# Performance work log

Measured on AMD Instinct MI355X. Metric: run time of the kernel, lower is better.

Reference implementation:

```python
import jax, jax.numpy as jnp
import numpy as np

N_AA = 300000
N_PROT = 30000
D_AA = 128
D_PROT = 128
HID = 128
OUT = 64
E_AP = 300000
E_PP = 960000
BATCH = 16384
NEG_SLOPE = 0.2


def _gatv2(x_src, x_dst, src, dst, Wl, bl, Wr, br, att, bias, num_dst):
    # GATv2Conv (heads=1): e_ij = att . leaky_relu(Wl x_j + Wr x_i); softmax over dst; out_i = sum alpha_ij * (Wl x_j) + bias
    xl = x_src @ Wl + bl                      # [Ns, C]
    xr = x_dst @ Wr + br                      # [Nd, C]
    e = jax.nn.leaky_relu(xl[src] + xr[dst], NEG_SLOPE)   # [E, C]
    logits = e @ att                          # [E]
    lmax = jax.ops.segment_max(logits, dst, num_segments=num_dst)
    ex = jnp.exp(logits - lmax[dst])
    denom = jax.ops.segment_sum(ex, dst, num_segments=num_dst)
    alpha = ex / denom[dst]                   # [E]
    msg = xl[src] * alpha[:, None]            # [E, C]
    out = jax.ops.segment_sum(msg, dst, num_segments=num_dst)
    return out + bias


def setup_inputs() -> dict:
    key = jax.random.key(0)
    ks = jax.random.split(key, 16)
    s = 0.05
    x_aa = jax.random.normal(ks[0], (N_AA, D_AA), jnp.float32)
    x_prot = jax.random.normal(ks[1], (N_PROT, D_PROT), jnp.float32)
    edge_index_ap = jnp.stack([
        jax.random.randint(ks[2], (E_AP,), 0, N_AA),
        jax.random.randint(ks[3], (E_AP,), 0, N_PROT)])
    edge_index_pp = jnp.stack([
        jax.random.randint(ks[4], (E_PP,), 0, N_PROT),
        jax.random.randint(ks[5], (E_PP,), 0, N_PROT)])
    return {
        'x_aa': x_aa, 'x_prot': x_prot,
        'edge_index_ap': edge_index_ap, 'edge_index_pp': edge_index_pp,
        'batch_size': BATCH,
        'Wl_ap': s * jax.random.normal(ks[6], (D_AA, HID), jnp.float32),
        'bl_ap': jnp.zeros((HID,), jnp.float32),
        'Wr_ap': s * jax.random.normal(ks[7], (D_PROT, HID), jnp.float32),
        'br_ap': jnp.zeros((HID,), jnp.float32),
        'att_ap': s * jax.random.normal(ks[8], (HID,), jnp.float32),
        'bias_ap': jnp.zeros((HID,), jnp.float32),
        'Wl_pp': s * jax.random.normal(ks[9], (D_PROT, HID), jnp.float32),
        'bl_pp': jnp.zeros((HID,), jnp.float32),
        'Wr_pp': s * jax.random.normal(ks[10], (D_PROT, HID), jnp.float32),
        'br_pp': jnp.zeros((HID,), jnp.float32),
        'att_pp': s * jax.random.normal(ks[11], (HID,), jnp.float32),
        'bias_pp': jnp.zeros((HID,), jnp.float32),
        'W_lin': s * jax.random.normal(ks[12], (HID, OUT), jnp.float32),
        'b_lin': jnp.zeros((OUT,), jnp.float32),
    }


def reference(x_aa, x_prot, edge_index_ap, edge_index_pp, batch_size,
              Wl_ap, bl_ap, Wr_ap, br_ap, att_ap, bias_ap,
              Wl_pp, bl_pp, Wr_pp, br_pp, att_pp, bias_pp,
              W_lin, b_lin):
    out_ap = _gatv2(x_aa, x_prot, edge_index_ap[0], edge_index_ap[1],
                    Wl_ap, bl_ap, Wr_ap, br_ap, att_ap, bias_ap, N_PROT)
    out_pp = _gatv2(x_prot, x_prot, edge_index_pp[0], edge_index_pp[1],
                    Wl_pp, bl_pp, Wr_pp, br_pp, att_pp, bias_pp, N_PROT)
    x = out_ap + out_pp                      # HeteroConv aggr='sum'
    x = jax.nn.relu(x[:batch_size])
    return x @ W_lin + b_lin
```

## Files before the change

kernel.cpp:

```cpp
#include <hip/hip_runtime.h>
#include <hip/hip_bf16.h>

typedef __attribute__((ext_vector_type(8))) short short8;
typedef __attribute__((ext_vector_type(4))) unsigned short ushort4_t;
typedef __attribute__((ext_vector_type(4))) float f32x4;

#define CAP_AP 64
#define CAP_PP 128

__device__ __forceinline__ unsigned short f2bf(float f) {
  unsigned u = __float_as_uint(f);
  u += 0x7FFFu + ((u >> 16) & 1u);
  return (unsigned short)(u >> 16);
}

__global__ __launch_bounds__(256) void k_init(
    int* __restrict__ map, int* __restrict__ cnt_ap, int* __restrict__ cnt_pp,
    int* __restrict__ ccount, int n_aa, int batch)
{
  int i = blockIdx.x * 256 + threadIdx.x;
  if (i < n_aa) map[i] = -1;
  if (i < batch) { cnt_ap[i] = 0; cnt_pp[i] = 0; }
  if (i == 0) *ccount = 0;
}

__global__ __launch_bounds__(256) void k_edges(
    const int* __restrict__ ei_ap, const int* __restrict__ ei_pp,
    int* __restrict__ map, int* __restrict__ cnt_ap, int* __restrict__ cnt_pp,
    int* __restrict__ csr_ap, int* __restrict__ csr_pp,
    int e_ap, int e_pp, int nb_ap, int batch)
{
  int b = blockIdx.x;
  if (b < nb_ap) {
    int e = b * 256 + threadIdx.x;
    if (e < e_ap) {
      int d = ei_ap[e_ap + e];
      if (d < batch) {
        int s = ei_ap[e];
        int pos = atomicAdd(&cnt_ap[d], 1);
        if (pos < CAP_AP) csr_ap[d * CAP_AP + pos] = s;
        map[s] = 1;
      }
    }
  } else {
    int e = (b - nb_ap) * 256 + threadIdx.x;
    if (e < e_pp) {
      int d = ei_pp[e_pp + e];
      if (d < batch) {
        int pos = atomicAdd(&cnt_pp[d], 1);
        if (pos < CAP_PP) csr_pp[d * CAP_PP + pos] = ei_pp[e];
      }
    }
  }
}

__global__ __launch_bounds__(256) void k_assign(
    int* __restrict__ map, int* __restrict__ inv, int* __restrict__ ccount, int n)
{
  __shared__ int wb[4];
  int i = blockIdx.x * 256 + threadIdx.x;
  bool need = (i < n) && (map[i] == 1);
  unsigned long long m = __ballot(need);
  int wave = threadIdx.x >> 6;
  int lane = threadIdx.x & 63;
  if (lane == 0) wb[wave] = __popcll(m);
  __syncthreads();
  if (threadIdx.x == 0) {
    int t0 = wb[0], t1 = wb[1], t2 = wb[2], t3 = wb[3];
    int tot = t0 + t1 + t2 + t3;
    int base = tot ? atomicAdd(ccount, tot) : 0;
    wb[0] = base;
    wb[1] = base + t0;
    wb[2] = base + t0 + t1;
    wb[3] = base + t0 + t1 + t2;
  }
  __syncthreads();
  if (need) {
    int slot = wb[wave] + __popcll(m & ((1ull << lane) - 1ull));
    map[i] = slot;
    inv[slot] = i;
  }
}

struct GemmJob {
  const float* X; const int* inv; const int* rowsp; int M;
  const float* W; const float* bias; unsigned short* Y; int nb;
};

__device__ __forceinline__ void gemm_body(const GemmJob& J, int bid, short8* lwb)
{
  const int tid = threadIdx.x;
  const int rows = J.rowsp ? *J.rowsp : J.M;
  const int wave = tid >> 6;
  const int lane = tid & 63;
  const int quad = lane >> 4;
  const int l16  = lane & 15;

  int tile = bid;
  long xrow = -1;
  float4 xa[4], xb[4];
  {
    int ra = tile * 64 + wave * 16 + l16;
    if (ra < rows) xrow = J.inv ? (long)J.inv[ra] : (long)ra;
    if (xrow >= 0) {
#pragma unroll
      for (int kt = 0; kt < 4; ++kt) {
        const float* p = J.X + xrow * 128 + kt * 32 + quad * 8;
        xa[kt] = ((const float4*)p)[0];
        xb[kt] = ((const float4*)p)[1];
      }
    }
  }

  {
    unsigned short* lw16 = (unsigned short*)lwb;
#pragma unroll
    for (int p = 0; p < 16; ++p) {
      int fi = p * 1024 + tid * 4;
      float4 w4 = *(const float4*)(J.W + fi);
#pragma unroll
      for (int q = 0; q < 4; ++q) {
        int k = (fi + q) >> 7, n = (fi + q) & 127;
        float wv = (q == 0) ? w4.x : (q == 1) ? w4.y : (q == 2) ? w4.z : w4.w;
        int e = ((k >> 5) * 8 + (n >> 4)) * 64 + ((k >> 3) & 3) * 16 + (n & 15);
        e ^= (e >> 6) & 7;
        lw16[e * 8 + (k & 7)] = f2bf(wv);
      }
    }
  }
  __syncthreads();

  for (; tile * 64 < rows; tile += J.nb) {
    int ra = tile * 64 + wave * 16 + l16;
    if (tile != bid) {
      xrow = -1;
      if (ra < rows) xrow = J.inv ? (long)J.inv[ra] : (long)ra;
      if (xrow >= 0) {
#pragma unroll
        for (int kt = 0; kt < 4; ++kt) {
          const float* p = J.X + xrow * 128 + kt * 32 + quad * 8;
          xa[kt] = ((const float4*)p)[0];
          xb[kt] = ((const float4*)p)[1];
        }
      }
    }

    short8 xf[4];
#pragma unroll
    for (int kt = 0; kt < 4; ++kt) {
      short8 a = {};
      if (xrow >= 0) {
        a[0] = (short)f2bf(xa[kt].x); a[1] = (short)f2bf(xa[kt].y);
        a[2] = (short)f2bf(xa[kt].z); a[3] = (short)f2bf(xa[kt].w);
        a[4] = (short)f2bf(xb[kt].x); a[5] = (short)f2bf(xb[kt].y);
        a[6] = (short)f2bf(xb[kt].z); a[7] = (short)f2bf(xb[kt].w);
      }
      xf[kt] = a;
    }

    f32x4 accs[8];
#pragma unroll
    for (int nt = 0; nt < 8; ++nt) {
      f32x4 acc = {0.f, 0.f, 0.f, 0.f};
#pragma unroll
      for (int kt = 0; kt < 4; ++kt)
        acc = __builtin_amdgcn_mfma_f32_16x16x32_bf16(
            lwb[(kt * 8 + nt) * 64 + (lane ^ nt)], xf[kt], acc, 0, 0, 0);
      accs[nt] = acc;
    }

    if (ra < rows) {
      unsigned short* yp = J.Y + (long)ra * 128;
#pragma unroll
      for (int nt = 0; nt < 8; ++nt) {
        int col = nt * 16 + quad * 4;
        float4 bv = *(const float4*)(J.bias + col);
        ushort4_t v;
        v[0] = f2bf(accs[nt][0] + bv.x);
        v[1] = f2bf(accs[nt][1] + bv.y);
        v[2] = f2bf(accs[nt][2] + bv.z);
        v[3] = f2bf(accs[nt][3] + bv.w);
        *(ushort4_t*)(yp + col) = v;
      }
    }
  }
}

__global__ __launch_bounds__(256) void k_mega(
    GemmJob j0, GemmJob j1, GemmJob j2, GemmJob j3,
    const int* __restrict__ map, const int* __restrict__ cnt_ap,
    int* __restrict__ csr_ap, int nb_gemm, int nb_remap, int batch)
{
  __shared__ short8 lwb[4 * 8 * 64];
  int b = blockIdx.x;
  if (b < nb_gemm) {
    if (b < j0.nb)                      gemm_body(j0, b, lwb);
    else if (b < j0.nb + j1.nb)         gemm_body(j1, b - j0.nb, lwb);
    else if (b < j0.nb + j1.nb + j2.nb) gemm_body(j2, b - j0.nb - j1.nb, lwb);
    else                                gemm_body(j3, b - j0.nb - j1.nb - j2.nb, lwb);
  } else {
    int i = (b - nb_gemm) * 256 + threadIdx.x;
    if (i < batch * CAP_AP) {
      int d = i / CAP_AP;
      int slot = i - d * CAP_AP;
      int n = cnt_ap[d]; if (n > CAP_AP) n = CAP_AP;
      if (slot < n) csr_ap[i] = map[csr_ap[i]];
    }
  }
}

__global__ __launch_bounds__(256) void k_gat_final(
    const int* __restrict__ cnt_ap, const int* __restrict__ csr_ap,
    const unsigned short* __restrict__ xl_aa,
    const unsigned short* __restrict__ xr_ap, const float* __restrict__ att_ap,
    const int* __restrict__ cnt_pp, const int* __restrict__ csr_pp,
    const unsigned short* __restrict__ xl_pp,
    const unsigned short* __restrict__ xr_pp, const float* __restrict__ att_pp,
    const float* __restrict__ bias_ap, const float* __restrict__ bias_pp,
    const float* __restrict__ W_lin, const float* __restrict__ b_lin,
    float* __restrict__ out, int batch)
{
  __shared__ unsigned lw2[64 * 64];
  __shared__ float lh[4][128];
  for (int e = threadIdx.x; e < 4096; e += 256) {
    int cp = e >> 6, o = e & 63;
    unsigned lo = f2bf(W_lin[(2 * cp) * 64 + o]);
    unsigned hi = f2bf(W_lin[(2 * cp + 1) * 64 + o]);
    lw2[e] = lo | (hi << 16);
  }

  const int wave = threadIdx.x >> 6;
  const int lane = threadIdx.x & 63;
  const int g    = lane >> 4;
  const int l16  = lane & 15;
  const int cb   = l16 * 8;
  const int dst  = blockIdx.x * 4 + wave;

  float h[8];
  if (dst < batch) {
    {
      float4 ba0 = *(const float4*)(bias_ap + cb);
      float4 ba1 = *(const float4*)(bias_ap + cb + 4);
      float4 bp0 = *(const float4*)(bias_pp + cb);
      float4 bp1 = *(const float4*)(bias_pp + cb + 4);
      h[0] = ba0.x + bp0.x; h[1] = ba0.y + bp0.y;
      h[2] = ba0.z + bp0.z; h[3] = ba0.w + bp0.w;
      h[4] = ba1.x + bp1.x; h[5] = ba1.y + bp1.y;
      h[6] = ba1.z + bp1.z; h[7] = ba1.w + bp1.w;
    }

#pragma unroll
    for (int type = 0; type < 2; ++type) {
      const int* cnt  = type ? cnt_pp : cnt_ap;
      const int* csr  = type ? csr_pp : csr_ap;
      const int cap   = type ? CAP_PP : CAP_AP;
      const unsigned short* xl = type ? xl_pp : xl_aa;
      const unsigned short* xr = type ? xr_pp : xr_ap;
      const float* att = type ? att_pp : att_ap;

      int n = __builtin_amdgcn_readfirstlane(cnt[dst]);
      if (n > cap) n = cap;
      const long base = (long)dst * cap;

      float xrv[8], atv[8];
      {
        short8 uxr = *(const short8*)(xr + (long)dst * 128 + cb);
#pragma unroll
        for (int k = 0; k < 8; ++k)
          xrv[k] = __uint_as_float(((unsigned)(unsigned short)uxr[k]) << 16);
        float4 a0 = *(const float4*)(att + cb);
        float4 a1 = *(const float4*)(att + cb + 4);
        atv[0] = a0.x; atv[1] = a0.y; atv[2] = a0.z; atv[3] = a0.w;
        atv[4] = a1.x; atv[5] = a1.y; atv[6] = a1.z; atv[7] = a1.w;
      }

      float l = 0.f, o[8];
#pragma unroll
      for (int k = 0; k < 8; ++k) o[k] = 0.f;

      if (n > 0) {
        bool act = g < n;
        int si = act ? csr[base + g] : 0;
        short8 ua = *(const short8*)(xl + (long)si * 128 + cb);
        int niter = (n + 3) >> 2;
        for (int it = 0; it < niter; ++it) {
          int en = it * 4 + 4 + g;
          bool actn = en < n;
          int sin = actn ? csr[base + en] : 0;
          short8 uan = *(const short8*)(xl + (long)sin * 128 + cb);

          float a[8];
#pragma unroll
          for (int k = 0; k < 8; ++k)
            a[k] = __uint_as_float(((unsigned)(unsigned short)ua[k]) << 16);
          float p = 0.f;
#pragma unroll
          for (int k = 0; k < 8; ++k) {
            float e = a[k] + xrv[k];
            e = e > 0.f ? e : 0.2f * e;
            p = fmaf(atv[k], e, p);
          }
          p += __shfl_xor(p, 8, 64);
          p += __shfl_xor(p, 4, 64);
          p += __shfl_xor(p, 2, 64);
          p += __shfl_xor(p, 1, 64);
          float w = act ? __expf(p) : 0.f;
          l += w;
#pragma unroll
          for (int k = 0; k < 8; ++k) o[k] = fmaf(w, a[k], o[k]);

          ua = uan; act = actn;
        }
      }
      l += __shfl_xor(l, 16, 64);
      l += __shfl_xor(l, 32, 64);
#pragma unroll
      for (int k = 0; k < 8; ++k) {
        o[k] += __shfl_xor(o[k], 16, 64);
        o[k] += __shfl_xor(o[k], 32, 64);
      }
      float invl = (l > 0.f) ? 1.f / l : 0.f;
#pragma unroll
      for (int k = 0; k < 8; ++k) h[k] = fmaf(o[k], invl, h[k]);
    }
  } else {
#pragma unroll
    for (int k = 0; k < 8; ++k) h[k] = 0.f;
  }

  if (g == 0) {
    float4 r0, r1;
    r0.x = h[0] > 0.f ? h[0] : 0.f; r0.y = h[1] > 0.f ? h[1] : 0.f;
    r0.z = h[2] > 0.f ? h[2] : 0.f; r0.w = h[3] > 0.f ? h[3] : 0.f;
    r1.x = h[4] > 0.f ? h[4] : 0.f; r1.y = h[5] > 0.f ? h[5] : 0.f;
    r1.z = h[6] > 0.f ? h[6] : 0.f; r1.w = h[7] > 0.f ? h[7] : 0.f;
    *(float4*)&lh[wave][cb]     = r0;
    *(float4*)&lh[wave][cb + 4] = r1;
  }
  __syncthreads();

  if (dst < batch) {
    float acc = b_lin[lane];
#pragma unroll 16
    for (int cp = 0; cp < 64; ++cp) {
      unsigned u = lw2[cp * 64 + lane];
      acc = fmaf(lh[wave][2 * cp],     __uint_as_float(u << 16),        acc);
      acc = fmaf(lh[wave][2 * cp + 1], __uint_as_float(u & 0xffff0000u), acc);
    }
    out[(long)dst * 64 + lane] = acc;
  }
}

extern "C" void kernel_launch(void* const* d_in, const int* in_sizes, int n_in,
                              void* d_out, int out_size, void* d_ws, size_t ws_size,
                              hipStream_t stream)
{
  const float* x_aa   = (const float*)d_in[0];
  const float* x_prot = (const float*)d_in[1];
  const int*   ei_ap  = (const int*)d_in[2];
  const int*   ei_pp  = (const int*)d_in[3];
  const float* Wl_ap  = (const float*)d_in[5];
  const float* bl_ap  = (const float*)d_in[6];
  const float* Wr_ap  = (const float*)d_in[7];
  const float* br_ap  = (const float*)d_in[8];
  const float* att_ap = (const float*)d_in[9];
  const float* bias_ap= (const float*)d_in[10];
  const float* Wl_pp  = (const float*)d_in[11];
  const float* bl_pp  = (const float*)d_in[12];
  const float* Wr_pp  = (const float*)d_in[13];
  const float* br_pp  = (const float*)d_in[14];
  const float* att_pp = (const float*)d_in[15];
  const float* bias_pp= (const float*)d_in[16];
  const float* W_lin  = (const float*)d_in[17];
  const float* b_lin  = (const float*)d_in[18];
  float* out = (float*)d_out;

  const int D = 128;
  const int n_aa   = in_sizes[0] / D;
  const int n_prot = in_sizes[1] / D;
  const int e_ap   = in_sizes[2] / 2;
  const int e_pp   = in_sizes[3] / 2;
  const int batch  = out_size / 64;

  char* p = (char*)d_ws;
  auto take = [&](size_t n) { char* r = p; p += (n + 255) & ~(size_t)255; return r; };
  unsigned short* xlc_aa = (unsigned short*)take((size_t)n_aa * D * 2);
  unsigned short* xl_pp  = (unsigned short*)take((size_t)n_prot * D * 2);
  unsigned short* xr_ap  = (unsigned short*)take((size_t)batch * D * 2);
  unsigned short* xr_pp  = (unsigned short*)take((size_t)batch * D * 2);
  int* map      = (int*)take((size_t)n_aa * 4);
  int* inv      = (int*)take((size_t)n_aa * 4);
  int* ccount   = (int*)take(4);
  int* cnt_ap   = (int*)take((size_t)batch * 4);
  int* cnt_pp   = (int*)take((size_t)batch * 4);
  int* csr_ap   = (int*)take((size_t)batch * CAP_AP * 4);
  int* csr_pp   = (int*)take((size_t)batch * CAP_PP * 4);
  (void)ws_size; (void)n_in;

  const int nb_ap = (e_ap + 255) / 256;
  const int nb_pp = (e_pp + 255) / 256;
  const int nb_init = (n_aa + 255) / 256;

  k_init<<<nb_init, 256, 0, stream>>>(map, cnt_ap, cnt_pp, ccount, n_aa, batch);
  k_edges<<<nb_ap + nb_pp, 256, 0, stream>>>(
      ei_ap, ei_pp, map, cnt_ap, cnt_pp, csr_ap, csr_pp,
      e_ap, e_pp, nb_ap, batch);
  k_assign<<<nb_init, 256, 0, stream>>>(map, inv, ccount, n_aa);

  GemmJob j0{x_aa,   inv,     ccount,  0,      Wl_ap, bl_ap, xlc_aa, 2560};
  GemmJob j1{x_prot, nullptr, nullptr, n_prot, Wl_pp, bl_pp, xl_pp,  (n_prot + 63) / 64};
  GemmJob j2{x_prot, nullptr, nullptr, batch,  Wr_ap, br_ap, xr_ap,  (batch + 63) / 64};
  GemmJob j3{x_prot, nullptr, nullptr, batch,  Wr_pp, br_pp, xr_pp,  (batch + 63) / 64};
  const int nb_gemm = j0.nb + j1.nb + j2.nb + j3.nb;
  const int nb_remap = (batch * CAP_AP + 255) / 256;
  k_mega<<<nb_gemm + nb_remap, 256, 0, stream>>>(
      j0, j1, j2, j3, map, cnt_ap, csr_ap, nb_gemm, nb_remap, batch);

  k_gat_final<<<(batch + 3) / 4, 256, 0, stream>>>(
      cnt_ap, csr_ap, xlc_aa, xr_ap, att_ap,
      cnt_pp, csr_pp, xl_pp, xr_pp, att_pp,
      bias_ap, bias_pp, W_lin, b_lin, out, batch);
}
```

Baseline: 419.0 us.

## Prefetch next tile's X rows in GEMM loop and use persistent block counts

The GEMM tile loop now loads the next tile's input rows into registers before computing the current tile, overlapping global loads with MFMA work and the bf16 stores. Block counts for the four GEMM jobs become fixed, smaller numbers, so each block loops over many tiles in a persistent style and the per-block weight staging into LDS is amortized. This raises register pressure from the extra prefetch buffers and cuts the number of blocks available to hide latency.

```diff
diff --git a/kernel.cpp b/kernel.cpp
--- a/kernel.cpp
+++ b/kernel.cpp
@@ -130,17 +130,21 @@
   }
   __syncthreads();
 
-  for (; tile * 64 < rows; tile += J.nb) {
-    int ra = tile * 64 + wave * 16 + l16;
-    if (tile != bid) {
-      xrow = -1;
-      if (ra < rows) xrow = J.inv ? (long)J.inv[ra] : (long)ra;
-      if (xrow >= 0) {
+  while (tile * 64 < rows) {
+    const int ra = tile * 64 + wave * 16 + l16;
+    const int tnext = tile + J.nb;
+
+    long xrow_n = -1;
+    float4 na[4], nb4[4];
+    if (tnext * 64 < rows) {
+      int rn = tnext * 64 + wave * 16 + l16;
+      if (rn < rows) xrow_n = J.inv ? (long)J.inv[rn] : (long)rn;
+      if (xrow_n >= 0) {
 #pragma unroll
         for (int kt = 0; kt < 4; ++kt) {
-          const float* p = J.X + xrow * 128 + kt * 32 + quad * 8;
-          xa[kt] = ((const float4*)p)[0];
-          xb[kt] = ((const float4*)p)[1];
+          const float* p = J.X + xrow_n * 128 + kt * 32 + quad * 8;
+          na[kt]  = ((const float4*)p)[0];
+          nb4[kt] = ((const float4*)p)[1];
         }
       }
     }
@@ -183,6 +187,11 @@
         *(ushort4_t*)(yp + col) = v;
       }
     }
+
+    xrow = xrow_n;
+#pragma unroll
+    for (int kt = 0; kt < 4; ++kt) { xa[kt] = na[kt]; xb[kt] = nb4[kt]; }
+    tile = tnext;
   }
 }
 
@@ -407,10 +416,10 @@
       e_ap, e_pp, nb_ap, batch);
   k_assign<<<nb_init, 256, 0, stream>>>(map, inv, ccount, n_aa);
 
-  GemmJob j0{x_aa,   inv,     ccount,  0,      Wl_ap, bl_ap, xlc_aa, 2560};
-  GemmJob j1{x_prot, nullptr, nullptr, n_prot, Wl_pp, bl_pp, xl_pp,  (n_prot + 63) / 64};
-  GemmJob j2{x_prot, nullptr, nullptr, batch,  Wr_ap, br_ap, xr_ap,  (batch + 63) / 64};
-  GemmJob j3{x_prot, nullptr, nullptr, batch,  Wr_pp, br_pp, xr_pp,  (batch + 63) / 64};
+  GemmJob j0{x_aa,   inv,     ccount,  0,      Wl_ap, bl_ap, xlc_aa, 512};
+  GemmJob j1{x_prot, nullptr, nullptr, n_prot, Wl_pp, bl_pp, xl_pp,  256};
+  GemmJob j2{x_prot, nullptr, nullptr, batch,  Wr_ap, br_ap, xr_ap,  128};
+  GemmJob j3{x_prot, nullptr, nullptr, batch,  Wr_pp, br_pp, xr_pp,  128};
   const int nb_gemm = j0.nb + j1.nb + j2.nb + j3.nb;
   const int nb_remap = (batch * CAP_AP + 255) / 256;
   k_mega<<<nb_gemm + nb_remap, 256, 0, stream>>>(
```

After: 408.3 us. 2.6% less time.
